# Kernel optimization log

Measured on AMD Instinct MI355X. Metric: run time of the kernel, lower is better.

## Reference

```python
import jax, jax.numpy as jnp
import numpy as np

B = 8192
T = 100       # repeat_vector
I = 30        # input_size
H = 100       # hidden_size


def setup_inputs() -> dict:
    key = jax.random.key(0)
    ks = jax.random.split(key, 7)
    k = 1.0 / np.sqrt(H)  # torch LSTM/Linear init scale
    u = lambda kk, shape: jax.random.uniform(kk, shape, jnp.float32, -k, k)
    return {
        "x": jax.random.normal(ks[0], (B, I), jnp.float32),
        "W_ih": u(ks[1], (4 * H, I)),   # gate order: i, f, g, o
        "W_hh": u(ks[2], (4 * H, H)),
        "b_ih": u(ks[3], (4 * H,)),
        "b_hh": u(ks[4], (4 * H,)),
        "W_d": u(ks[5], (1, H)),
        "b_d": u(ks[6], (1,)),
    }


def _lstm_dense(x, W_ih, W_hh, b_ih, b_hh, W_d, b_d):
    # Input is the same vector at every timestep (repeat), so project once.
    xp = x @ W_ih.T + b_ih + b_hh  # [B, 4H]
    h0 = jnp.zeros((x.shape[0], H), x.dtype)
    c0 = jnp.zeros((x.shape[0], H), x.dtype)

    def step(carry, _):
        h, c = carry
        gates = xp + h @ W_hh.T                      # [B, 4H]
        i, f, g, o = jnp.split(gates, 4, axis=-1)
        i = jax.nn.sigmoid(i)
        f = jax.nn.sigmoid(f)
        g = jnp.tanh(g)
        o = jax.nn.sigmoid(o)
        c = f * c + i * g
        h = o * jnp.tanh(c)
        return (h, c), h

    _, hs = jax.lax.scan(step, (h0, c0), None, length=T)  # [T, B, H]
    hs = jnp.transpose(hs, (1, 0, 2))                     # [B, T, H]
    return hs @ W_d.T + b_d                               # [B, T, 1]


def reference(x, W_ih, W_hh, b_ih, b_hh, W_d, b_d):
    return _lstm_dense(x, W_ih, W_hh, b_ih, b_hh, W_d, b_d)
```

## Files before the change

kernel.cpp:

```cpp
#include <hip/hip_runtime.h>


#define LOG2E 1.44269504088896340736f

typedef _Float16 f16x8 __attribute__((ext_vector_type(8)));
typedef float    f32x4 __attribute__((ext_vector_type(4)));
typedef float    f32x2 __attribute__((ext_vector_type(2)));

__device__ __forceinline__ float rcp_(float x) { return __builtin_amdgcn_rcpf(x); }
__device__ __forceinline__ float exp2_(float x) { return __builtin_amdgcn_exp2f(x); }

#define KS 136
#define XQR 288

__global__ __launch_bounds__(448, 4) void lstm_kernel(
    const float* __restrict__ x, const float* __restrict__ Wih,
    const float* __restrict__ Whh, const float* __restrict__ bih,
    const float* __restrict__ bhh, const float* __restrict__ Wd,
    const float* __restrict__ bd, float* __restrict__ out)
{
    __shared__ __align__(16) char smem[128 * KS * 2];
    __shared__ __align__(16) _Float16 hlds[2][16 * KS];
    __shared__ __align__(16) float xq_lds[7 * 4 * XQR];

    _Float16* Wstg = (_Float16*)smem;
    float*    outb = (float*)smem;

    const int tid = threadIdx.x;
    const int w   = tid >> 6;
    const int l   = tid & 63;
    const int g   = l >> 4;
    const int c   = l & 15;
    const int b0  = blockIdx.x * 16;
    const int u   = w * 16 + c;
    const bool wpo = (u == 101);

    for (int i = tid; i < 128 * KS / 2; i += 448) ((unsigned*)Wstg)[i] = 0u;
    for (int i = tid; i < 2 * 16 * KS / 2; i += 448) ((unsigned*)&hlds[0][0])[i] = 0u;
    __syncthreads();

    f16x8 wfrag[4][4];
    for (int s = 0; s < 4; ++s) {
        const float sc = (s == 2) ? (-2.0f * LOG2E) : (-LOG2E);
        for (int idx = tid; idx < 10000; idx += 448) {
            int uu = idx / 100, k = idx - uu * 100;
            Wstg[uu * KS + k] = (_Float16)(Whh[(s * 100 + uu) * 100 + k] * sc);
        }
        if (s == 0)
            for (int k = tid; k < 100; k += 448)
                Wstg[101 * KS + k] = (_Float16)Wd[k];
        __syncthreads();
        #pragma unroll
        for (int ks = 0; ks < 4; ++ks)
            wfrag[s][ks] = *(const f16x8*)&Wstg[u * KS + ks * 32 + g * 8];
        __syncthreads();
    }

    const int xqsw = l * 4 + ((l >> 3) << 2);
    {
        float xq[4][4];
        #pragma unroll
        for (int s = 0; s < 4; ++s)
            #pragma unroll
            for (int r = 0; r < 4; ++r) xq[s][r] = 0.0f;
        if (u < 100) {
            for (int k = 0; k < 30; ++k) {
                float xv[4];
                #pragma unroll
                for (int r = 0; r < 4; ++r) xv[r] = x[(b0 + 4 * g + r) * 30 + k];
                #pragma unroll
                for (int s = 0; s < 4; ++s) {
                    float wv = Wih[(s * 100 + u) * 30 + k];
                    #pragma unroll
                    for (int r = 0; r < 4; ++r) xq[s][r] += xv[r] * wv;
                }
            }
            #pragma unroll
            for (int s = 0; s < 4; ++s) {
                float sc = (s == 2) ? (-2.0f * LOG2E) : (-LOG2E);
                float b  = bih[s * 100 + u] + bhh[s * 100 + u];
                #pragma unroll
                for (int r = 0; r < 4; ++r) xq[s][r] = (xq[s][r] + b) * sc;
            }
        }
        #pragma unroll
        for (int s = 0; s < 4; ++s) {
            f32x4 v = {xq[s][0], xq[s][1], xq[s][2], xq[s][3]};
            *(f32x4*)&xq_lds[(w * 4 + s) * XQR + xqsw] = v;
        }
    }
    const float bdv = bd[0];
    f32x2 creg2[2] = {{0.f, 0.f}, {0.f, 0.f}};
    __syncthreads();

    const int afb = c * KS + g * 8;
    const int xqb = w * 4 * XQR + xqsw;

    f32x4 acc[4];
    #pragma unroll
    for (int s = 0; s < 4; ++s)
        acc[s] = *(const f32x4*)&xq_lds[xqb + s * XQR];
    __syncthreads();

#define STEP(P, TCUR)                                                         \
    {                                                                         \
        const _Float16* hr = &hlds[(P)][0];                                   \
        _Float16*       hw = &hlds[(P) ^ 1][0];                               \
        f16x8 af[4];                                                          \
        _Pragma("unroll")                                                     \
        for (int ks = 0; ks < 4; ++ks)                                        \
            af[ks] = *(const f16x8*)&hr[afb + ks * 32];                       \
        _Pragma("unroll")                                                     \
        for (int ks = 0; ks < 4; ++ks)                                        \
            _Pragma("unroll")                                                 \
            for (int s = 0; s < 4; ++s)                                       \
                acc[s] = __builtin_amdgcn_mfma_f32_16x16x32_f16(              \
                        af[ks], wfrag[s][ks], acc[s], 0, 0, 0);               \
                  \
        if ((TCUR) > 0 && wpo) {                                              \
            _Pragma("unroll")                                                 \
            for (int r = 0; r < 4; ++r)                                       \
                outb[(4 * g + r) * 100 + (TCUR) - 1] = acc[0][r] + bdv;       \
        }                                                                     \
                                   \
        _Pragma("unroll")                                                     \
        for (int q = 0; q < 2; ++q) {                                         \
            f32x2 A2 = {exp2_(acc[0][2 * q]), exp2_(acc[0][2 * q + 1])};      \
            f32x2 F2 = {exp2_(acc[1][2 * q]), exp2_(acc[1][2 * q + 1])};      \
            f32x2 G2 = {exp2_(acc[2][2 * q]), exp2_(acc[2][2 * q + 1])};      \
            f32x2 O2 = {exp2_(acc[3][2 * q]), exp2_(acc[3][2 * q + 1])};      \
            f32x2 a1 = A2 + 1.0f;                                             \
            f32x2 f1 = F2 + 1.0f;                                             \
            f32x2 g1 = G2 + 1.0f;                                             \
            f32x2 gm = 1.0f - G2;                                             \
            f32x2 ag = a1 * g1;                                               \
            f32x2 num = creg2[q] * ag + gm * f1;                              \
            f32x2 den = ag * f1;                                              \
            f32x2 rd = {rcp_(den[0]), rcp_(den[1])};                          \
            f32x2 cg = num * rd;                                              \
            creg2[q] = cg;                                                    \
            f32x2 cgk = cg * (-2.0f * LOG2E);                                 \
            f32x2 C2 = {exp2_(cgk[0]), exp2_(cgk[1])};                        \
            f32x2 c2m = 1.0f - C2;                                            \
            f32x2 od = (O2 + 1.0f) * (C2 + 1.0f);                             \
            f32x2 ro = {rcp_(od[0]), rcp_(od[1])};                            \
            f32x2 hv = c2m * ro;                                              \
            hw[(4 * g + 2 * q) * KS + u]     = (_Float16)hv[0];               \
            hw[(4 * g + 2 * q + 1) * KS + u] = (_Float16)hv[1];               \
        }                                                                     \
                  \
        _Pragma("unroll")                                                     \
        for (int s = 0; s < 4; ++s)                                           \
            acc[s] = *(const f32x4*)&xq_lds[xqb + s * XQR];                   \
        __syncthreads();                                                      \
    }

    for (int t2 = 0; t2 < 50; ++t2) {
        STEP(0, 2 * t2);
        STEP(1, 2 * t2 + 1);
    }
#undef STEP

    {
        f32x4 a99 = {0.f, 0.f, 0.f, 0.f};
        #pragma unroll
        for (int ks = 0; ks < 4; ++ks) {
            f16x8 a = *(const f16x8*)&hlds[0][afb + ks * 32];
            a99 = __builtin_amdgcn_mfma_f32_16x16x32_f16(a, wfrag[0][ks], a99, 0, 0, 0);
        }
        if (wpo) {
            #pragma unroll
            for (int r = 0; r < 4; ++r)
                outb[(4 * g + r) * 100 + 99] = a99[r] + bdv;
        }
    }
    __syncthreads();

    {
        f32x4*       o4 = (f32x4*)(out + b0 * 100);
        const f32x4* s4 = (const f32x4*)outb;
        for (int i = tid; i < 400; i += 448) o4[i] = s4[i];
    }
}

extern "C" void kernel_launch(void* const* d_in, const int* in_sizes, int n_in,
                              void* d_out, int out_size, void* d_ws, size_t ws_size,
                              hipStream_t stream) {
    (void)in_sizes; (void)n_in; (void)out_size; (void)d_ws; (void)ws_size;
    const float* x   = (const float*)d_in[0];
    const float* Wih = (const float*)d_in[1];
    const float* Whh = (const float*)d_in[2];
    const float* bih = (const float*)d_in[3];
    const float* bhh = (const float*)d_in[4];
    const float* Wd  = (const float*)d_in[5];
    const float* bd  = (const float*)d_in[6];
    lstm_kernel<<<dim3(512), dim3(448), 0, stream>>>(
        x, Wih, Whh, bih, bhh, Wd, bd, (float*)d_out);
}
```

Before: 138.7 us.

## Interleave two independent batch tiles per block to hide recurrence latency

Each block now handles 32 batch rows as two independent 16-row LSTM chains (X and Y) and alternates phases between them. Each phase prefetches the next chain's h fragments before its barrier, so one chain's MFMA and gate math can overlap the other's LDS round trip. Input projections stay in registers instead of being reloaded from LDS every step, and the grid is halved to 256 blocks with launch bounds lowered to 2 blocks per SM. The cost is more registers, fewer blocks to spread across CUs, twice as many barriers per block, and a scalar output store in place of vectorised stores.

```diff
diff --git a/kernel.cpp b/kernel.cpp
--- a/kernel.cpp
+++ b/kernel.cpp
@@ -11,32 +11,31 @@
 __device__ __forceinline__ float exp2_(float x) { return __builtin_amdgcn_exp2f(x); }
 
 #define KS 136
-#define XQR 288
-
-__global__ __launch_bounds__(448, 4) void lstm_kernel(
+
+__global__ __launch_bounds__(448, 2) void lstm_kernel(
     const float* __restrict__ x, const float* __restrict__ Wih,
     const float* __restrict__ Whh, const float* __restrict__ bih,
     const float* __restrict__ bhh, const float* __restrict__ Wd,
     const float* __restrict__ bd, float* __restrict__ out)
 {
     __shared__ __align__(16) char smem[128 * KS * 2];
-    __shared__ __align__(16) _Float16 hlds[2][16 * KS];
-    __shared__ __align__(16) float xq_lds[7 * 4 * XQR];
-
-    _Float16* Wstg = (_Float16*)smem;
-    float*    outb = (float*)smem;
+    __shared__ __align__(16) _Float16 hlds[4][16 * KS];
+
+    _Float16* Wstg  = (_Float16*)smem;
+    float*    outbX = (float*)smem;
+    float*    outbY = (float*)smem + 1600;
 
     const int tid = threadIdx.x;
     const int w   = tid >> 6;
     const int l   = tid & 63;
     const int g   = l >> 4;
     const int c   = l & 15;
-    const int b0  = blockIdx.x * 16;
+    const int b0  = blockIdx.x * 32;
     const int u   = w * 16 + c;
     const bool wpo = (u == 101);
 
     for (int i = tid; i < 128 * KS / 2; i += 448) ((unsigned*)Wstg)[i] = 0u;
-    for (int i = tid; i < 2 * 16 * KS / 2; i += 448) ((unsigned*)&hlds[0][0])[i] = 0u;
+    for (int i = tid; i < 4 * 16 * KS / 2; i += 448) ((unsigned*)&hlds[0][0])[i] = 0u;
     __syncthreads();
 
     f16x8 wfrag[4][4];
@@ -56,73 +55,71 @@
         __syncthreads();
     }
 
-    const int xqsw = l * 4 + ((l >> 3) << 2);
-    {
-        float xq[4][4];
-        #pragma unroll
-        for (int s = 0; s < 4; ++s)
-            #pragma unroll
-            for (int r = 0; r < 4; ++r) xq[s][r] = 0.0f;
-        if (u < 100) {
-            for (int k = 0; k < 30; ++k) {
-                float xv[4];
+    f32x4 xqX[4], xqY[4];
+    #pragma unroll
+    for (int s = 0; s < 4; ++s) {
+        xqX[s] = (f32x4){0.f, 0.f, 0.f, 0.f};
+        xqY[s] = (f32x4){0.f, 0.f, 0.f, 0.f};
+    }
+    if (u < 100) {
+        for (int k = 0; k < 30; ++k) {
+            float xvX[4], xvY[4];
+            #pragma unroll
+            for (int r = 0; r < 4; ++r) {
+                xvX[r] = x[(b0 + 4 * g + r) * 30 + k];
+                xvY[r] = x[(b0 + 16 + 4 * g + r) * 30 + k];
+            }
+            #pragma unroll
+            for (int s = 0; s < 4; ++s) {
+                float wv = Wih[(s * 100 + u) * 30 + k];
                 #pragma unroll
-                for (int r = 0; r < 4; ++r) xv[r] = x[(b0 + 4 * g + r) * 30 + k];
-                #pragma unroll
-                for (int s = 0; s < 4; ++s) {
-                    float wv = Wih[(s * 100 + u) * 30 + k];
-                    #pragma unroll
-                    for (int r = 0; r < 4; ++r) xq[s][r] += xv[r] * wv;
+                for (int r = 0; r < 4; ++r) {
+                    xqX[s][r] += xvX[r] * wv;
+                    xqY[s][r] += xvY[r] * wv;
                 }
             }
-            #pragma unroll
-            for (int s = 0; s < 4; ++s) {
-                float sc = (s == 2) ? (-2.0f * LOG2E) : (-LOG2E);
-                float b  = bih[s * 100 + u] + bhh[s * 100 + u];
-                #pragma unroll
-                for (int r = 0; r < 4; ++r) xq[s][r] = (xq[s][r] + b) * sc;
+        }
+        #pragma unroll
+        for (int s = 0; s < 4; ++s) {
+            float sc = (s == 2) ? (-2.0f * LOG2E) : (-LOG2E);
+            float b  = bih[s * 100 + u] + bhh[s * 100 + u];
+            #pragma unroll
+            for (int r = 0; r < 4; ++r) {
+                xqX[s][r] = (xqX[s][r] + b) * sc;
+                xqY[s][r] = (xqY[s][r] + b) * sc;
             }
         }
-        #pragma unroll
-        for (int s = 0; s < 4; ++s) {
-            f32x4 v = {xq[s][0], xq[s][1], xq[s][2], xq[s][3]};
-            *(f32x4*)&xq_lds[(w * 4 + s) * XQR + xqsw] = v;
-        }
     }
     const float bdv = bd[0];
-    f32x2 creg2[2] = {{0.f, 0.f}, {0.f, 0.f}};
+    f32x2 cregX[2] = {{0.f, 0.f}, {0.f, 0.f}};
+    f32x2 cregY[2] = {{0.f, 0.f}, {0.f, 0.f}};
+
+    const int afb = c * KS + g * 8;
+
+    f16x8 afp[4];
+    #pragma unroll
+    for (int ks = 0; ks < 4; ++ks)
+        afp[ks] = *(const f16x8*)&hlds[0][afb + ks * 32];
     __syncthreads();
 
-    const int afb = c * KS + g * 8;
-    const int xqb = w * 4 * XQR + xqsw;
-
-    f32x4 acc[4];
-    #pragma unroll
-    for (int s = 0; s < 4; ++s)
-        acc[s] = *(const f32x4*)&xq_lds[xqb + s * XQR];
-    __syncthreads();
-
-#define STEP(P, TCUR)                                                         \
+#define PHASE(WR, PF, XQ, CREG, OUTB, TCUR)                                   \
     {                                                                         \
-        const _Float16* hr = &hlds[(P)][0];                                   \
-        _Float16*       hw = &hlds[(P) ^ 1][0];                               \
-        f16x8 af[4];                                                          \
-        _Pragma("unroll")                                                     \
-        for (int ks = 0; ks < 4; ++ks)                                        \
-            af[ks] = *(const f16x8*)&hr[afb + ks * 32];                       \
-        _Pragma("unroll")                                                     \
-        for (int ks = 0; ks < 4; ++ks)                                        \
+        f32x4 acc[4];                                                         \
+        _Pragma("unroll")                                                     \
+        for (int s = 0; s < 4; ++s)                                           \
+            acc[s] = __builtin_amdgcn_mfma_f32_16x16x32_f16(                  \
+                    afp[0], wfrag[s][0], XQ[s], 0, 0, 0);                     \
+        _Pragma("unroll")                                                     \
+        for (int ks = 1; ks < 4; ++ks)                                        \
             _Pragma("unroll")                                                 \
             for (int s = 0; s < 4; ++s)                                       \
                 acc[s] = __builtin_amdgcn_mfma_f32_16x16x32_f16(              \
-                        af[ks], wfrag[s][ks], acc[s], 0, 0, 0);               \
-                  \
+                        afp[ks], wfrag[s][ks], acc[s], 0, 0, 0);              \
         if ((TCUR) > 0 && wpo) {                                              \
             _Pragma("unroll")                                                 \
             for (int r = 0; r < 4; ++r)                                       \
-                outb[(4 * g + r) * 100 + (TCUR) - 1] = acc[0][r] + bdv;       \
+                OUTB[(4 * g + r) * 100 + (TCUR) - 1] = acc[0][r] + bdv;       \
         }                                                                     \
-                                   \
         _Pragma("unroll")                                                     \
         for (int q = 0; q < 2; ++q) {                                         \
             f32x2 A2 = {exp2_(acc[0][2 * q]), exp2_(acc[0][2 * q + 1])};      \
@@ -134,52 +131,66 @@
             f32x2 g1 = G2 + 1.0f;                                             \
             f32x2 gm = 1.0f - G2;                                             \
             f32x2 ag = a1 * g1;                                               \
-            f32x2 num = creg2[q] * ag + gm * f1;                              \
+            f32x2 num = CREG[q] * ag + gm * f1;                               \
             f32x2 den = ag * f1;                                              \
             f32x2 rd = {rcp_(den[0]), rcp_(den[1])};                          \
             f32x2 cg = num * rd;                                              \
-            creg2[q] = cg;                                                    \
+            CREG[q] = cg;                                                     \
             f32x2 cgk = cg * (-2.0f * LOG2E);                                 \
             f32x2 C2 = {exp2_(cgk[0]), exp2_(cgk[1])};                        \
             f32x2 c2m = 1.0f - C2;                                            \
             f32x2 od = (O2 + 1.0f) * (C2 + 1.0f);                             \
             f32x2 ro = {rcp_(od[0]), rcp_(od[1])};                            \
             f32x2 hv = c2m * ro;                                              \
-            hw[(4 * g + 2 * q) * KS + u]     = (_Float16)hv[0];               \
-            hw[(4 * g + 2 * q + 1) * KS + u] = (_Float16)hv[1];               \
+            (WR)[(4 * g + 2 * q) * KS + u]     = (_Float16)hv[0];             \
+            (WR)[(4 * g + 2 * q + 1) * KS + u] = (_Float16)hv[1];             \
         }                                                                     \
-                  \
-        _Pragma("unroll")                                                     \
-        for (int s = 0; s < 4; ++s)                                           \
-            acc[s] = *(const f32x4*)&xq_lds[xqb + s * XQR];                   \
+        _Pragma("unroll")                                                     \
+        for (int ks = 0; ks < 4; ++ks)                                        \
+            afp[ks] = *(const f16x8*)&(PF)[afb + ks * 32];                    \
         __syncthreads();                                                      \
     }
 
     for (int t2 = 0; t2 < 50; ++t2) {
-        STEP(0, 2 * t2);
-        STEP(1, 2 * t2 + 1);
-    }
-#undef STEP
+        const int t0 = 2 * t2, t1 = 2 * t2 + 1;
+        PHASE(&hlds[1][0], &hlds[2][0], xqX, cregX, outbX, t0)
+        PHASE(&hlds[3][0], &hlds[1][0], xqY, cregY, outbY, t0)
+        PHASE(&hlds[0][0], &hlds[3][0], xqX, cregX, outbX, t1)
+        PHASE(&hlds[2][0], &hlds[0][0], xqY, cregY, outbY, t1)
+    }
+#undef PHASE
 
     {
         f32x4 a99 = {0.f, 0.f, 0.f, 0.f};
         #pragma unroll
+        for (int ks = 0; ks < 4; ++ks)
+            a99 = __builtin_amdgcn_mfma_f32_16x16x32_f16(
+                    afp[ks], wfrag[0][ks], a99, 0, 0, 0);
+        if (wpo) {
+            #pragma unroll
+            for (int r = 0; r < 4; ++r)
+                outbX[(4 * g + r) * 100 + 99] = a99[r] + bdv;
+        }
+    }
+    {
+        f32x4 a99 = {0.f, 0.f, 0.f, 0.f};
+        #pragma unroll
         for (int ks = 0; ks < 4; ++ks) {
-            f16x8 a = *(const f16x8*)&hlds[0][afb + ks * 32];
+            f16x8 a = *(const f16x8*)&hlds[2][afb + ks * 32];
             a99 = __builtin_amdgcn_mfma_f32_16x16x32_f16(a, wfrag[0][ks], a99, 0, 0, 0);
         }
         if (wpo) {
             #pragma unroll
             for (int r = 0; r < 4; ++r)
-                outb[(4 * g + r) * 100 + 99] = a99[r] + bdv;
+                outbY[(4 * g + r) * 100 + 99] = a99[r] + bdv;
         }
     }
     __syncthreads();
 
     {
-        f32x4*       o4 = (f32x4*)(out + b0 * 100);
-        const f32x4* s4 = (const f32x4*)outb;
-        for (int i = tid; i < 400; i += 448) o4[i] = s4[i];
+        const float* s4 = (const float*)smem;
+        for (int i = tid; i < 3200; i += 448)
+            out[b0 * 100 + i] = s4[i];
     }
 }
 
@@ -194,6 +205,6 @@
     const float* bhh = (const float*)d_in[4];
     const float* Wd  = (const float*)d_in[5];
     const float* bd  = (const float*)d_in[6];
-    lstm_kernel<<<dim3(512), dim3(448), 0, stream>>>(
+    lstm_kernel<<<dim3(256), dim3(448), 0, stream>>>(
         x, Wih, Whh, bih, bhh, Wd, bd, (float*)d_out);
 }
```

Result: slower. 147.9 us (+6.6%).
